# Performance work log

Measured on AMD Instinct MI355X. Metric: run time of the kernel, lower is better.

Reference implementation:

```python
import jax, jax.numpy as jnp
import numpy as np

EPROJS = 512
ODIM = 600
DLAYERS = 2
DUNITS = 512
EMBED_DIM = 512
JOINT_DIM = 512
BLANK = 0


def setup_inputs() -> dict:
    key = jax.random.key(0)
    ks = jax.random.split(key, 20)
    B, T, U = 16, 200, 64
    s_d = 1.0 / np.sqrt(DUNITS)
    s_e = 1.0 / np.sqrt(EPROJS)
    s_j = 1.0 / np.sqrt(JOINT_DIM)
    inp = {
        "hs_pad": jax.random.normal(ks[0], (B, T, EPROJS), dtype=jnp.float32),
        "ys_in_pad": jax.random.randint(ks[1], (B, U), 0, ODIM),
        "embed_table": jax.random.normal(ks[2], (ODIM, EMBED_DIM), dtype=jnp.float32).at[BLANK].set(0.0),
        # LSTMCell layer 0: input EMBED_DIM -> DUNITS (gates i,f,g,o stacked => 4*DUNITS)
        "W_ih0": jax.random.uniform(ks[3], (4 * DUNITS, EMBED_DIM), minval=-s_d, maxval=s_d),
        "W_hh0": jax.random.uniform(ks[4], (4 * DUNITS, DUNITS), minval=-s_d, maxval=s_d),
        "b_ih0": jax.random.uniform(ks[5], (4 * DUNITS,), minval=-s_d, maxval=s_d),
        "b_hh0": jax.random.uniform(ks[6], (4 * DUNITS,), minval=-s_d, maxval=s_d),
        # LSTMCell layer 1: DUNITS -> DUNITS
        "W_ih1": jax.random.uniform(ks[7], (4 * DUNITS, DUNITS), minval=-s_d, maxval=s_d),
        "W_hh1": jax.random.uniform(ks[8], (4 * DUNITS, DUNITS), minval=-s_d, maxval=s_d),
        "b_ih1": jax.random.uniform(ks[9], (4 * DUNITS,), minval=-s_d, maxval=s_d),
        "b_hh1": jax.random.uniform(ks[10], (4 * DUNITS,), minval=-s_d, maxval=s_d),
        # joint network
        "W_enc": jax.random.uniform(ks[11], (JOINT_DIM, EPROJS), minval=-s_e, maxval=s_e),
        "b_enc": jax.random.uniform(ks[12], (JOINT_DIM,), minval=-s_e, maxval=s_e),
        "W_dec": jax.random.uniform(ks[13], (JOINT_DIM, DUNITS), minval=-s_d, maxval=s_d),
        "W_out": jax.random.uniform(ks[14], (ODIM, JOINT_DIM), minval=-s_j, maxval=s_j),
        "b_out": jax.random.uniform(ks[15], (ODIM,), minval=-s_j, maxval=s_j),
    }
    return inp


def _lstm_cell(x, h, c, W_ih, W_hh, b_ih, b_hh):
    gates = x @ W_ih.T + b_ih + h @ W_hh.T + b_hh  # (B, 4*D)
    i, f, g, o = jnp.split(gates, 4, axis=-1)
    c_new = jax.nn.sigmoid(f) * c + jax.nn.sigmoid(i) * jnp.tanh(g)
    h_new = jax.nn.sigmoid(o) * jnp.tanh(c_new)
    return h_new, c_new


def _decode(eys, W_ih0, W_hh0, b_ih0, b_hh0, W_ih1, W_hh1, b_ih1, b_hh1):
    # eys: (B, U, E). Sequential 2-layer LSTM over U via scan.
    B = eys.shape[0]
    z = jnp.zeros((B, DUNITS), dtype=eys.dtype)
    carry0 = (z, z, z, z)  # h0, c0, h1, c1

    def step(carry, ey):
        h0, c0, h1, c1 = carry
        h0, c0 = _lstm_cell(ey, h0, c0, W_ih0, W_hh0, b_ih0, b_hh0)
        h1, c1 = _lstm_cell(h0, h1, c1, W_ih1, W_hh1, b_ih1, b_hh1)
        return (h0, c0, h1, c1), h1

    _, h_dec = jax.lax.scan(step, carry0, jnp.swapaxes(eys, 0, 1))  # (U, B, D)
    return jnp.swapaxes(h_dec, 0, 1)  # (B, U, D)


def reference(hs_pad, ys_in_pad, embed_table, W_ih0, W_hh0, b_ih0, b_hh0,
              W_ih1, W_hh1, b_ih1, b_hh1, W_enc, b_enc, W_dec, W_out, b_out):
    eys = embed_table[ys_in_pad]  # (B, U, E); dropout = identity at p=0
    h_dec = _decode(eys, W_ih0, W_hh0, b_ih0, b_hh0, W_ih1, W_hh1, b_ih1, b_hh1)
    # Joint: project BEFORE broadcasting (thin GEMMs), then broadcast-add.
    enc_p = hs_pad @ W_enc.T + b_enc            # (B, T, J)
    dec_p = h_dec @ W_dec.T                     # (B, U, J)
    z = jnp.tanh(enc_p[:, :, None, :] + dec_p[:, None, :, :])  # (B, T, U, J)
    return z @ W_out.T + b_out                  # (B, T, U, odim)
```

## Files before the change

kernel.cpp:

```cpp
#include <hip/hip_runtime.h>
#include <hip/hip_bf16.h>
#include <stdint.h>

#define DEVI __device__ __forceinline__

typedef unsigned short u16;
typedef __attribute__((ext_vector_type(8))) short short8;
typedef __attribute__((ext_vector_type(4))) float f32x4;
typedef __attribute__((ext_vector_type(16))) float f32x16;

DEVI u16 f2bf(float f) {
  union { float f; uint32_t u; } v; v.f = f;
  return (u16)((v.u + 0x7fffu + ((v.u >> 16) & 1u)) >> 16);
}
DEVI float tanh_c(float x) {
  float e = __expf(x + x);
  float r = __builtin_amdgcn_rcpf(e + 1.0f);
  return __builtin_fmaf(-2.0f, r, 1.0f);
}
DEVI float sigm(float x) { return __builtin_amdgcn_rcpf(1.0f + __expf(-x)); }
DEVI uint32_t tj2(float a, float b) {
  float ea = __expf(a + a), eb = __expf(b + b);
  float ta = __builtin_fmaf(-2.0f, __builtin_amdgcn_rcpf(ea + 1.0f), 1.0f);
  float tb = __builtin_fmaf(-2.0f, __builtin_amdgcn_rcpf(eb + 1.0f), 1.0f);
  union { __hip_bfloat162 h; uint32_t u; } cv;
  cv.h = __float22bfloat162_rn(make_float2(ta, tb));
  return cv.u;
}

__global__ void prep_kernel(
    const float* __restrict__ W_ih0, const float* __restrict__ W_hh0,
    const float* __restrict__ W_ih1, const float* __restrict__ W_hh1,
    const float* __restrict__ W_enc, const float* __restrict__ W_dec,
    const float* __restrict__ W_out, const float* __restrict__ embed,
    const float* __restrict__ hs_pad,
    const float* __restrict__ b_ih0, const float* __restrict__ b_hh0,
    const float* __restrict__ b_ih1, const float* __restrict__ b_hh1,
    const float* __restrict__ b_out,
    u16* __restrict__ Wih0b, u16* __restrict__ Whh0b,
    u16* __restrict__ Wih1b, u16* __restrict__ Whh1b,
    u16* __restrict__ Wencb, u16* __restrict__ Wdecb,
    u16* __restrict__ embedb, u16* __restrict__ hsb,
    u16* __restrict__ Wshufb,
    float* __restrict__ bsum0, float* __restrict__ bsum1, float* __restrict__ boutp)
{
  const int c1 = 1048576, c2 = 2097152, c3 = 3145728, c4 = 4194304;
  const int c5 = 4456448, c6 = 4718592, c7 = 5025792, c8 = 6664192;
  const int c9 = 6991872, c10 = 6993920, c11 = 6995968, c12 = 6996608;
  for (int i = blockIdx.x * blockDim.x + threadIdx.x; i < c12; i += gridDim.x * blockDim.x) {
    if (i < c1)       Wih0b[i]      = f2bf(W_ih0[i]);
    else if (i < c2)  Whh0b[i - c1] = f2bf(W_hh0[i - c1]);
    else if (i < c3)  Wih1b[i - c2] = f2bf(W_ih1[i - c2]);
    else if (i < c4)  Whh1b[i - c3] = f2bf(W_hh1[i - c3]);
    else if (i < c5)  Wencb[i - c4] = f2bf(W_enc[i - c4]);
    else if (i < c6)  Wdecb[i - c5] = f2bf(W_dec[i - c5]);
    else if (i < c7)  embedb[i - c6] = f2bf(embed[i - c6]);
    else if (i < c8)  hsb[i - c7]   = f2bf(hs_pad[i - c7]);
    else if (i < c9) {
      int e = i - c8;
      int kc = e / 10240, r = e % 10240;
      int tile = r >> 9, r2 = r & 511;
      int lane = r2 >> 3, ii = r2 & 7;
      int n = tile * 32 + (lane & 31);
      int k = kc * 16 + ((lane >> 5) << 3) + ii;
      Wshufb[e] = (n < 600) ? f2bf(W_out[n * 512 + k]) : (u16)0;
    }
    else if (i < c10) { int n = i - c9;  bsum0[n] = b_ih0[n] + b_hh0[n]; }
    else if (i < c11) { int n = i - c10; bsum1[n] = b_ih1[n] + b_hh1[n]; }
    else              { int n = i - c11; boutp[n] = (n < 600) ? b_out[n] : 0.0f; }
  }
}

__global__ __launch_bounds__(256) void gemm_bf16(
    const u16* __restrict__ A, const u16* __restrict__ B,
    const int* __restrict__ ys, const float* __restrict__ bias,
    float* __restrict__ out, int N, int mode)
{
  int tid = threadIdx.x, wv = tid >> 6, l = tid & 63;
  int m0 = blockIdx.x * 64, n0 = blockIdx.y * 64;
  int row = m0 + wv * 16 + (l & 15);
  const u16* arow;
  if (mode == 1) { int uu = row >> 4, bb = row & 15; arow = A + (size_t)ys[bb * 64 + uu] * 512; }
  else           arow = A + (size_t)row * 512;
  int kof = (l >> 4) * 8;
  arow += kof;
  const u16* br = B + (size_t)(n0 + (l & 15)) * 512 + kof;
  f32x4 a0 = {0.f,0.f,0.f,0.f}, a1 = a0, a2 = a0, a3 = a0;
  for (int kk = 0; kk < 512; kk += 32) {
    short8 av = *(const short8*)(arow + kk);
    short8 b0 = *(const short8*)(br + kk);
    short8 b1 = *(const short8*)(br + 8192 + kk);
    short8 b2 = *(const short8*)(br + 16384 + kk);
    short8 b3 = *(const short8*)(br + 24576 + kk);
    a0 = __builtin_amdgcn_mfma_f32_16x16x32_bf16(av, b0, a0, 0, 0, 0);
    a1 = __builtin_amdgcn_mfma_f32_16x16x32_bf16(av, b1, a1, 0, 0, 0);
    a2 = __builtin_amdgcn_mfma_f32_16x16x32_bf16(av, b2, a2, 0, 0, 0);
    a3 = __builtin_amdgcn_mfma_f32_16x16x32_bf16(av, b3, a3, 0, 0, 0);
  }
  int col = l & 15, rb = m0 + wv * 16 + (l >> 4) * 4;
  f32x4 accs[4] = {a0, a1, a2, a3};
#pragma unroll
  for (int g = 0; g < 4; ++g) {
    int n = n0 + g * 16 + col;
    float bs = bias ? bias[n] : 0.0f;
#pragma unroll
    for (int i2 = 0; i2 < 4; ++i2)
      out[(size_t)(rb + i2) * N + n] = accs[g][i2] + bs;
  }
}

#define L0WG 32
#define NWGT 96

DEVI short8 ald16(const u16* p) {
  union { unsigned long long q[2]; short8 v; } u;
  u.q[0] = __hip_atomic_load((unsigned long long*)p,       __ATOMIC_RELAXED, __HIP_MEMORY_SCOPE_AGENT);
  u.q[1] = __hip_atomic_load((unsigned long long*)(p + 4), __ATOMIC_RELAXED, __HIP_MEMORY_SCOPE_AGENT);
  return u.v;
}
DEVI void waitflags(const int* f0, const int* f1, int n0, int n1) {
  if (threadIdx.x < 64) {
    int l = threadIdx.x;
    for (;;) {
      int a = __hip_atomic_load((int*)(f0 + (l & 31) * 16), __ATOMIC_RELAXED, __HIP_MEMORY_SCOPE_AGENT);
      int b = __hip_atomic_load((int*)(f1 + l * 16),        __ATOMIC_RELAXED, __HIP_MEMORY_SCOPE_AGENT);
      if (__all(a >= n0 && b >= n1)) break;
      __builtin_amdgcn_s_sleep(1);
    }
    __builtin_amdgcn_fence(__ATOMIC_ACQUIRE, "agent");
  }
  __syncthreads();
}
DEVI void postflag(int* slot, int val) {
  __syncthreads();
  if (threadIdx.x == 0) {
    asm volatile("s_waitcnt vmcnt(0)" ::: "memory");
    __hip_atomic_store(slot, val, __ATOMIC_RELAXED, __HIP_MEMORY_SCOPE_AGENT);
  }
}
DEVI const u16* haddr(const u16* base, int slot, int k, int b) {
  return base + slot * 8192 + (k >> 4) * 256 + b * 16 + (k & 15);
}
DEVI void hstore(u16* base, int idx, u16 mine, int tid) {
  int other = __shfl_xor((int)mine, 1);
  if (!(tid & 1)) {
    uint32_t pkv = (uint32_t)mine | (((uint32_t)other & 0xffffu) << 16);
    __hip_atomic_store((uint32_t*)(base + idx), pkv, __ATOMIC_RELAXED, __HIP_MEMORY_SCOPE_AGENT);
  }
}

__global__ __launch_bounds__(256) void lstm_kernel(
    const float* __restrict__ Xg0,
    const u16* __restrict__ Whh0, const u16* __restrict__ Wih1, const u16* __restrict__ Whh1,
    const float* __restrict__ bsum1,
    u16* __restrict__ h0b, u16* __restrict__ h1b,
    u16* __restrict__ Hdec,
    int* __restrict__ flags0, int* __restrict__ flags1)
{
  __shared__ float red[16][256];
  const int bid = blockIdx.x, tid = threadIdx.x;
  const int wv = tid >> 6, l = tid & 63;
  const int lb = l & 15, kof = (l >> 4) * 8;
  const int drb = (l >> 4) * 4;

  if (bid < L0WG) {
    const int be = tid >> 4, je = tid & 15, jg = (bid << 4) + je;
    short8 breg[16];
#pragma unroll
    for (int g = 0; g < 4; ++g) {
      const u16* bp = Whh0 + (size_t)(g * 512 + bid * 16 + lb) * 512 + wv * 128 + kof;
#pragma unroll
      for (int ks = 0; ks < 4; ++ks)
        breg[g * 4 + ks] = *(const short8*)(bp + ks * 32);
    }
    float c0 = 0.f;
    for (int t = 0; t < 64; ++t) {
      const float* xg = Xg0 + (size_t)((t << 4) + be) * 2048 + jg;
      float x0 = xg[0], x1 = xg[512], x2 = xg[1024], x3 = xg[1536];
      waitflags(flags0, flags1, t, (t > 7) ? (t - 7) : 0);
      const int rs = (t + 7) & 7;
      f32x4 g0 = {0.f,0.f,0.f,0.f}, g1 = g0, g2 = g0, g3 = g0;
#pragma unroll
      for (int ks = 0; ks < 4; ++ks) {
        int kk = wv * 128 + ks * 32 + kof;
        short8 av = ald16(haddr(h0b, rs, kk, lb));
        g0 = __builtin_amdgcn_mfma_f32_16x16x32_bf16(av, breg[0 * 4 + ks], g0, 0, 0, 0);
        g1 = __builtin_amdgcn_mfma_f32_16x16x32_bf16(av, breg[1 * 4 + ks], g1, 0, 0, 0);
        g2 = __builtin_amdgcn_mfma_f32_16x16x32_bf16(av, breg[2 * 4 + ks], g2, 0, 0, 0);
        g3 = __builtin_amdgcn_mfma_f32_16x16x32_bf16(av, breg[3 * 4 + ks], g3, 0, 0, 0);
      }
      f32x4 gs[4] = {g0, g1, g2, g3};
#pragma unroll
      for (int g = 0; g < 4; ++g)
#pragma unroll
        for (int i2 = 0; i2 < 4; ++i2)
          red[wv * 4 + g][(drb + i2) * 16 + lb] = gs[g][i2];
      __syncthreads();
      {
        float s0 = 0, s1 = 0, s2 = 0, s3 = 0;
#pragma unroll
        for (int v2 = 0; v2 < 4; ++v2) {
          s0 += red[v2 * 4 + 0][be * 16 + je]; s1 += red[v2 * 4 + 1][be * 16 + je];
          s2 += red[v2 * 4 + 2][be * 16 + je]; s3 += red[v2 * 4 + 3][be * 16 + je];
        }
        float gi = s0 + x0, gf = s1 + x1, gg = s2 + x2, go = s3 + x3;
        float I = sigm(gi), F = sigm(gf), G = tanh_c(gg), O = sigm(go);
        c0 = F * c0 + I * G;
        float h0 = O * tanh_c(c0);
        hstore(h0b, ((t & 7) * 32 + bid) * 256 + (tid & ~1), f2bf(h0), tid);
      }
      postflag(flags0 + bid * 16, t + 1);
    }
  } else {
    const int v = bid - L0WG;
    const u16* base0 = (wv < 2) ? Wih1 : Whh1;
    const int kbase = (wv & 1) * 256;
    short8 breg[16];
#pragma unroll
    for (int tt = 0; tt < 2; ++tt) {
      int c = tt * 16 + lb, gate = c >> 3, du = c & 7;
      const u16* bp = base0 + (size_t)(gate * 512 + v * 8 + du) * 512 + kbase + kof;
#pragma unroll
      for (int ks = 0; ks < 8; ++ks)
        breg[tt * 8 + ks] = *(const short8*)(bp + ks * 32);
    }
    float bs0 = 0, bs1 = 0, bs2 = 0, bs3 = 0, c1 = 0.f;
    if (tid < 128) {
      int du = tid & 7, ju = v * 8 + du;
      bs0 = bsum1[ju]; bs1 = bsum1[512 + ju]; bs2 = bsum1[1024 + ju]; bs3 = bsum1[1536 + ju];
    }
    for (int t = 0; t < 64; ++t) {
      waitflags(flags0, flags1, t + 1, t);
      const u16* hsrc = (wv < 2) ? (h0b + (t & 7) * 8192) : (h1b + ((t + 7) & 7) * 8192);
      f32x4 g0 = {0.f,0.f,0.f,0.f}, g1 = g0;
#pragma unroll
      for (int ks = 0; ks < 8; ++ks) {
        int kk = kbase + ks * 32 + kof;
        short8 av = ald16(hsrc + (kk >> 4) * 256 + lb * 16 + (kk & 15));
        g0 = __builtin_amdgcn_mfma_f32_16x16x32_bf16(av, breg[0 * 8 + ks], g0, 0, 0, 0);
        g1 = __builtin_amdgcn_mfma_f32_16x16x32_bf16(av, breg[1 * 8 + ks], g1, 0, 0, 0);
      }
#pragma unroll
      for (int i2 = 0; i2 < 4; ++i2) {
        red[wv * 2 + 0][(drb + i2) * 16 + lb] = g0[i2];
        red[wv * 2 + 1][(drb + i2) * 16 + lb] = g1[i2];
      }
      __syncthreads();
      u16 hb = 0; int be = 0, ju = 0;
      if (tid < 128) {
        be = tid >> 3; int du = tid & 7; ju = v * 8 + du;
        float sg[4] = {bs0, bs1, bs2, bs3};
#pragma unroll
        for (int g = 0; g < 4; ++g) {
          int c = g * 8 + du, tt = c >> 4, cc = c & 15;
          float acc = 0.f;
#pragma unroll
          for (int w2 = 0; w2 < 4; ++w2) acc += red[w2 * 2 + tt][be * 16 + cc];
          sg[g] += acc;
        }
        float I = sigm(sg[0]), F = sigm(sg[1]), G = tanh_c(sg[2]), O = sigm(sg[3]);
        c1 = F * c1 + I * G;
        float h1v = O * tanh_c(c1);
        hb = f2bf(h1v);
        int idx = ((t & 7) * 32 + (ju >> 4)) * 256 + be * 16 + (ju & 15);
        hstore(h1b, idx & ~1, hb, tid);
      }
      postflag(flags1 + v * 16, t + 1);
      if (tid < 128) Hdec[(size_t)((t << 4) + be) * 512 + ju] = hb;
    }
  }
}

__global__ __launch_bounds__(256) void joint_kernel(
    const float* __restrict__ enc_p,
    const float* __restrict__ dec_p,
    const u16* __restrict__ Wshuf,
    const float* __restrict__ boutp,
    float* __restrict__ out)
{
  __shared__ int4 wlds[2][1280];
  __shared__ int4 zlds[2][256];
  int bid = blockIdx.x;
  int b = bid / 400, rem = bid % 400;
  int tb = rem / 8, rem2 = rem % 8;
  int ub = rem2 >> 1, nh = rem2 & 1;
  int tid = threadIdx.x, wv = tid >> 6, l = tid & 63;
  int mv = wv >> 1, nv = wv & 1;
  int ln31 = l & 31, lh = l >> 5;
  const int tile0 = nv * 5;
  f32x16 acc[5];
#pragma unroll
  for (int j = 0; j < 5; ++j) {
    float bv = boutp[nh * 320 + (tile0 + j) * 32 + ln31];
#pragma unroll
    for (int g = 0; g < 16; ++g) acc[j][g] = bv;
  }
  int zr = tid & 63, zg = tid >> 6;
  const float* er = enc_p + (size_t)(b * 200 + tb * 4 + (zr >> 4)) * 512 + zg * 8;
  const float* dr = dec_p + (size_t)((ub * 16 + (zr & 15)) * 16 + b) * 512 + zg * 8;
  const int zslot = ((zg >> 1) * 2 + (zr >> 5)) * 64 + ((zg & 1) << 5) + (zr & 31);
  const int4* gW = (const int4*)Wshuf;
  const int nhof = nh * 640;
  const int L0 = tid, L1 = 256 + tid, L2 = 512 + tid + ((tid >= 128) ? 640 : 0),
            L3 = 1408 + tid, L4 = 1664 + tid;
  const int S2 = 512 + tid;

  {
    int4 w0 = gW[nhof + L0], w1 = gW[nhof + L1], w2 = gW[nhof + L2],
         w3 = gW[nhof + L3], w4 = gW[nhof + L4];
    float4 e0 = *(const float4*)(er),     e1 = *(const float4*)(er + 4);
    float4 d0 = *(const float4*)(dr),     d1 = *(const float4*)(dr + 4);
    int4 pk;
    pk.x = (int)tj2(e0.x + d0.x, e0.y + d0.y);
    pk.y = (int)tj2(e0.z + d0.z, e0.w + d0.w);
    pk.z = (int)tj2(e1.x + d1.x, e1.y + d1.y);
    pk.w = (int)tj2(e1.z + d1.z, e1.w + d1.w);
    zlds[0][zslot] = pk;
    wlds[0][tid] = w0; wlds[0][256 + tid] = w1; wlds[0][S2] = w2;
    wlds[0][768 + tid] = w3; wlds[0][1024 + tid] = w4;
    __syncthreads();
  }

  for (int c = 0; c < 16; ++c) {
    const int cur = c & 1, nxt = cur ^ 1;
    const bool pf = (c < 15);
    int4 w0, w1, w2, w3, w4;
    float4 e0, e1, d0, d1;
    if (pf) {
      const int cb = (c + 1) * 2560 + nhof;
      w0 = gW[cb + L0]; w1 = gW[cb + L1]; w2 = gW[cb + L2];
      w3 = gW[cb + L3]; w4 = gW[cb + L4];
      int k0 = (c + 1) * 32;
      e0 = *(const float4*)(er + k0);     e1 = *(const float4*)(er + k0 + 4);
      d0 = *(const float4*)(dr + k0);     d1 = *(const float4*)(dr + k0 + 4);
    }
#pragma unroll
    for (int ks = 0; ks < 2; ++ks) {
      short8 aA = *(const short8*)&zlds[cur][(ks * 2 + mv) * 64 + l];
#pragma unroll
      for (int j = 0; j < 5; ++j) {
        short8 bw = *(const short8*)&wlds[cur][ks * 640 + (tile0 + j) * 64 + l];
        acc[j] = __builtin_amdgcn_mfma_f32_32x32x16_bf16(aA, bw, acc[j], 0, 0, 0);
      }
    }
    if (pf) {
      wlds[nxt][tid] = w0; wlds[nxt][256 + tid] = w1; wlds[nxt][S2] = w2;
      wlds[nxt][768 + tid] = w3; wlds[nxt][1024 + tid] = w4;
      int4 pk;
      pk.x = (int)tj2(e0.x + d0.x, e0.y + d0.y);
      pk.y = (int)tj2(e0.z + d0.z, e0.w + d0.w);
      pk.z = (int)tj2(e1.x + d1.x, e1.y + d1.y);
      pk.w = (int)tj2(e1.z + d1.z, e1.w + d1.w);
      zlds[nxt][zslot] = pk;
    }
    __syncthreads();
  }

#pragma unroll
  for (int j = 0; j < 5; ++j) {
    int n = nh * 320 + (tile0 + j) * 32 + ln31;
    if (n < 600) {
      int rbase = mv * 32 + 4 * lh;
#pragma unroll
      for (int g = 0; g < 16; ++g) {
        int r = rbase + (g & 3) + ((g >> 2) << 3);
        int tt = tb * 4 + (r >> 4), uu = ub * 16 + (r & 15);
        out[(size_t)((b * 200 + tt) * 64 + uu) * 600 + n] = acc[j][g];
      }
    }
  }
}

extern "C" void kernel_launch(void* const* d_in, const int* in_sizes, int n_in,
                              void* d_out, int out_size, void* d_ws, size_t ws_size,
                              hipStream_t stream) {
  const float* hs_pad = (const float*)d_in[0];
  const int*   ys     = (const int*)d_in[1];
  const float* embed  = (const float*)d_in[2];
  const float* W_ih0  = (const float*)d_in[3];
  const float* W_hh0  = (const float*)d_in[4];
  const float* b_ih0  = (const float*)d_in[5];
  const float* b_hh0  = (const float*)d_in[6];
  const float* W_ih1  = (const float*)d_in[7];
  const float* W_hh1  = (const float*)d_in[8];
  const float* b_ih1  = (const float*)d_in[9];
  const float* b_hh1  = (const float*)d_in[10];
  const float* W_enc  = (const float*)d_in[11];
  const float* b_enc  = (const float*)d_in[12];
  const float* W_dec  = (const float*)d_in[13];
  const float* W_out  = (const float*)d_in[14];
  const float* b_out  = (const float*)d_in[15];
  float* out = (float*)d_out;

  uint8_t* ws = (uint8_t*)d_ws;
  size_t off = 0;
  auto alloc = [&](size_t bytes) -> void* {
    void* p = ws + off;
    off = (off + bytes + 255) & ~(size_t)255;
    return p;
  };
  int* flags0   = (int*)alloc(2048);
  int* flags1   = (int*)alloc(4096);
  u16* h0buf    = (u16*)alloc(8 * 32 * 256 * 2);
  u16* h1buf    = (u16*)alloc(8 * 32 * 256 * 2);
  u16* Hdec     = (u16*)alloc(64 * 16 * 512 * 2);
  float* Xg0    = (float*)alloc(1024 * 2048 * 4);
  float* enc_p  = (float*)alloc(3200 * 512 * 4);
  float* dec_p  = (float*)alloc(1024 * 512 * 4);
  u16* Wih0b    = (u16*)alloc(2048 * 512 * 2);
  u16* Whh0b    = (u16*)alloc(2048 * 512 * 2);
  u16* Wih1b    = (u16*)alloc(2048 * 512 * 2);
  u16* Whh1b    = (u16*)alloc(2048 * 512 * 2);
  u16* Wencb    = (u16*)alloc(512 * 512 * 2);
  u16* Wdecb    = (u16*)alloc(512 * 512 * 2);
  u16* embedb   = (u16*)alloc(600 * 512 * 2);
  u16* hsb      = (u16*)alloc(3200 * 512 * 2);
  u16* Wshufb   = (u16*)alloc(32 * 20 * 64 * 8 * 2);
  float* bsum0  = (float*)alloc(2048 * 4);
  float* bsum1  = (float*)alloc(2048 * 4);
  float* boutp  = (float*)alloc(640 * 4);

  (void)hipMemsetAsync(d_ws, 0, 2048 + 4096 + 131072 + 131072, stream);

  prep_kernel<<<2048, 256, 0, stream>>>(
      W_ih0, W_hh0, W_ih1, W_hh1, W_enc, W_dec, W_out, embed, hs_pad,
      b_ih0, b_hh0, b_ih1, b_hh1, b_out,
      Wih0b, Whh0b, Wih1b, Whh1b, Wencb, Wdecb, embedb, hsb, Wshufb,
      bsum0, bsum1, boutp);

  dim3 g1(16, 32);
  gemm_bf16<<<g1, 256, 0, stream>>>(embedb, Wih0b, ys, bsum0, Xg0, 2048, 1);
  dim3 g2(50, 8);
  gemm_bf16<<<g2, 256, 0, stream>>>(hsb, Wencb, nullptr, b_enc, enc_p, 512, 0);
  lstm_kernel<<<NWGT, 256, 0, stream>>>(Xg0, Whh0b, Wih1b, Whh1b, bsum1,
                                        h0buf, h1buf, Hdec, flags0, flags1);
  dim3 g3(16, 8);
  gemm_bf16<<<g3, 256, 0, stream>>>(Hdec, Wdecb, nullptr, nullptr, dec_p, 512, 0);
  joint_kernel<<<6400, 256, 0, stream>>>(enc_p, dec_p, Wshufb, boutp, out);
}
```

Measured before the change: 619.7 us.

## Stage joint weights via direct global-to-LDS loads and remap block order

Replaces the register-staged weight prefetch in the joint kernel with global_load_lds (16-byte) transfers straight into the shared double buffer, removing the VGPR round trip and the LDS store instructions. It also remaps blockIdx so consecutive blocks are spread across groups of 800 (likely to spread work across XCDs for L2 locality of the shared weights). This relies on the 16-byte global_load_lds placing data at the wave base plus lane offset, which must match the old layout. There is also a synchronisation risk: the direct loads must be complete before the barrier that precedes their use.

```diff
diff --git a/kernel.cpp b/kernel.cpp
--- a/kernel.cpp
+++ b/kernel.cpp
@@ -26,6 +26,11 @@
   union { __hip_bfloat162 h; uint32_t u; } cv;
   cv.h = __float22bfloat162_rn(make_float2(ta, tb));
   return cv.u;
+}
+DEVI void gl16(const int4* g, int4* l) {
+  __builtin_amdgcn_global_load_lds(
+      (const __attribute__((address_space(1))) uint32_t*)g,
+      (__attribute__((address_space(3))) uint32_t*)l, 16, 0, 0);
 }
 
 __global__ void prep_kernel(
@@ -280,7 +285,7 @@
 {
   __shared__ int4 wlds[2][1280];
   __shared__ int4 zlds[2][256];
-  int bid = blockIdx.x;
+  int bid = ((int)blockIdx.x & 7) * 800 + ((int)blockIdx.x >> 3);
   int b = bid / 400, rem = bid % 400;
   int tb = rem / 8, rem2 = rem % 8;
   int ub = rem2 >> 1, nh = rem2 & 1;
@@ -301,38 +306,40 @@
   const int zslot = ((zg >> 1) * 2 + (zr >> 5)) * 64 + ((zg & 1) << 5) + (zr & 31);
   const int4* gW = (const int4*)Wshuf;
   const int nhof = nh * 640;
-  const int L0 = tid, L1 = 256 + tid, L2 = 512 + tid + ((tid >= 128) ? 640 : 0),
-            L3 = 1408 + tid, L4 = 1664 + tid;
-  const int S2 = 512 + tid;
+  const int wvb = wv * 64;
+  const int s2g = (wv >= 2) ? 640 : 0;
+
+  auto stage_w = [&](int c, int buf) {
+    const int4* src = gW + c * 2560 + nhof;
+    gl16(src + tid,              &wlds[buf][wvb]);
+    gl16(src + 256 + tid,        &wlds[buf][256 + wvb]);
+    gl16(src + 512 + tid + s2g,  &wlds[buf][512 + wvb]);
+    gl16(src + 1408 + tid,       &wlds[buf][768 + wvb]);
+    gl16(src + 1664 + tid,       &wlds[buf][1024 + wvb]);
+  };
 
   {
-    int4 w0 = gW[nhof + L0], w1 = gW[nhof + L1], w2 = gW[nhof + L2],
-         w3 = gW[nhof + L3], w4 = gW[nhof + L4];
     float4 e0 = *(const float4*)(er),     e1 = *(const float4*)(er + 4);
     float4 d0 = *(const float4*)(dr),     d1 = *(const float4*)(dr + 4);
+    stage_w(0, 0);
     int4 pk;
     pk.x = (int)tj2(e0.x + d0.x, e0.y + d0.y);
     pk.y = (int)tj2(e0.z + d0.z, e0.w + d0.w);
     pk.z = (int)tj2(e1.x + d1.x, e1.y + d1.y);
     pk.w = (int)tj2(e1.z + d1.z, e1.w + d1.w);
     zlds[0][zslot] = pk;
-    wlds[0][tid] = w0; wlds[0][256 + tid] = w1; wlds[0][S2] = w2;
-    wlds[0][768 + tid] = w3; wlds[0][1024 + tid] = w4;
     __syncthreads();
   }
 
   for (int c = 0; c < 16; ++c) {
     const int cur = c & 1, nxt = cur ^ 1;
     const bool pf = (c < 15);
-    int4 w0, w1, w2, w3, w4;
     float4 e0, e1, d0, d1;
     if (pf) {
-      const int cb = (c + 1) * 2560 + nhof;
-      w0 = gW[cb + L0]; w1 = gW[cb + L1]; w2 = gW[cb + L2];
-      w3 = gW[cb + L3]; w4 = gW[cb + L4];
       int k0 = (c + 1) * 32;
       e0 = *(const float4*)(er + k0);     e1 = *(const float4*)(er + k0 + 4);
       d0 = *(const float4*)(dr + k0);     d1 = *(const float4*)(dr + k0 + 4);
+      stage_w(c + 1, nxt);
     }
 #pragma unroll
     for (int ks = 0; ks < 2; ++ks) {
@@ -344,8 +351,6 @@
       }
     }
     if (pf) {
-      wlds[nxt][tid] = w0; wlds[nxt][256 + tid] = w1; wlds[nxt][S2] = w2;
-      wlds[nxt][768 + tid] = w3; wlds[nxt][1024 + tid] = w4;
       int4 pk;
       pk.x = (int)tj2(e0.x + d0.x, e0.y + d0.y);
       pk.y = (int)tj2(e0.z + d0.z, e0.w + d0.w);
```

New measurement: 672.3 us. 8.5% more time.
